# Performance work log

Hardware: AMD Instinct MI355X
Metric: run time of the kernel (lower is better)

The kernel has to match this reference:

```python
import jax, jax.numpy as jnp
import numpy as np

N = 8192
IN_F = 512
OUT_F = 512


def setup_inputs() -> dict:
    key = jax.random.key(0)
    k1, k2, k3, k4, k5 = jax.random.split(key, 5)
    scale = 1.0 / np.sqrt(IN_F)
    return {
        "embedding": jax.random.normal(k1, (N, IN_F), dtype=jnp.float32),
        "W_qk": jax.random.uniform(k2, (OUT_F, IN_F), dtype=jnp.float32, minval=-scale, maxval=scale),
        "b_qk": jax.random.uniform(k3, (OUT_F,), dtype=jnp.float32, minval=-scale, maxval=scale),
        "W_v": jax.random.uniform(k4, (OUT_F, IN_F), dtype=jnp.float32, minval=-scale, maxval=scale),
        "b_v": jax.random.uniform(k5, (OUT_F,), dtype=jnp.float32, minval=-scale, maxval=scale),
    }


def reference(embedding, W_qk, b_qk, W_v, b_v):
    # Q and K share the same projection (query_key Linear)
    Q = embedding @ W_qk.T + b_qk          # [N, D]
    K = Q                                   # identical projection
    V = embedding @ W_v.T + b_v             # [N, D]
    inv_sqrt_d = 1.0 / jnp.sqrt(jnp.asarray(OUT_F, dtype=embedding.dtype))
    scores = (Q @ K.T) * inv_sqrt_d         # [N, N]
    attn = jax.nn.softmax(scores, axis=1)   # row-wise softmax (dim=1)
    return attn @ V                         # [N, D]
```

## Files before the change

### kernel.cpp

```cpp
#include <hip/hip_runtime.h>
#include <hip/hip_bf16.h>


#define NTOK 8192
#define DIM  512

typedef unsigned short ushort_t;
typedef __attribute__((ext_vector_type(8))) __bf16 bf16x8;
typedef __attribute__((ext_vector_type(4))) float f32x4;

__device__ __forceinline__ float bf2f(ushort_t u) {
    union { unsigned int i; float f; } v; v.i = ((unsigned int)u) << 16; return v.f;
}
__device__ __forceinline__ ushort_t f2bf(float f) {
    union { float f; unsigned int i; } v; v.f = f;
    unsigned int b = v.i;
    return (ushort_t)((b + 0x7FFFu + ((b >> 16) & 1u)) >> 16);
}
__device__ __forceinline__ __bf16 f2bfh(float f) {
    union { ushort_t u; __bf16 h; } c; c.u = f2bf(f); return c.h;
}
__device__ __forceinline__ f32x4 mfma16(bf16x8 a, bf16x8 b, f32x4 c) {
    return __builtin_amdgcn_mfma_f32_16x16x32_bf16(a, b, c, 0, 0, 0);
}
__device__ __forceinline__ bf16x8 load8(const void* p, size_t idx, bool f32) {
    if (f32) {
        const float* f = (const float*)p + idx;
        bf16x8 r;
        #pragma unroll
        for (int j = 0; j < 8; ++j) r[j] = f2bfh(f[j]);
        return r;
    }
    return *(const bf16x8*)((const ushort_t*)p + idx);
}
__device__ __forceinline__ float loadS(const void* p, size_t idx, bool f32) {
    return f32 ? ((const float*)p)[idx] : bf2f(((const ushort_t*)p)[idx]);
}

#define LDA 520
#define LDP 264

__global__ void detect_kernel(const ushort_t* __restrict__ emb, int* __restrict__ flag)
{
    int lane = threadIdx.x;
    int cnt = 0;
    #pragma unroll
    for (int i = 0; i < 8; ++i) {
        ushort_t u = emb[(size_t)(lane * 8 + i) * 2];
        int a = u & 0x7FFF;
        int e = (u >> 7) & 0xFF;
        if (a == 0 || (e >= 111 && e <= 143)) cnt++;
    }
    cnt += __shfl_xor(cnt, 1);  cnt += __shfl_xor(cnt, 2);  cnt += __shfl_xor(cnt, 4);
    cnt += __shfl_xor(cnt, 8);  cnt += __shfl_xor(cnt, 16); cnt += __shfl_xor(cnt, 32);
    if (lane == 0) *flag = (cnt >= 460) ? 1 : 0;
}

__global__ __launch_bounds__(256)
void prep_kernel(const int* __restrict__ flag,
                 const void* __restrict__ Wqk, const void* __restrict__ bqk,
                 const void* __restrict__ Wv,  const void* __restrict__ bv,
                 ushort_t* __restrict__ Wqkb, ushort_t* __restrict__ bqkb,
                 ushort_t* __restrict__ Wvb,  ushort_t* __restrict__ bvb)
{
    const bool f32 = (*flag == 0);
    size_t gid = (size_t)blockIdx.x * 256 + threadIdx.x;
    size_t base = gid * 8;
    *(bf16x8*)&Wqkb[base] = load8(Wqk, base, f32);
    *(bf16x8*)&Wvb[base]  = load8(Wv,  base, f32);
    if (gid < 64) {
        *(bf16x8*)&bqkb[base] = load8(bqk, base, f32);
        *(bf16x8*)&bvb[base]  = load8(bv,  base, f32);
    }
}

__global__ __launch_bounds__(512)
void projqT_kernel(const int* __restrict__ flag, const void* __restrict__ emb,
                   const ushort_t* __restrict__ Wb, const ushort_t* __restrict__ bb,
                   ushort_t* __restrict__ C, ushort_t* __restrict__ embT)
{
    __shared__ ushort_t Alds[64][LDA];
    const bool f32 = (*flag == 0);
    const int tid  = threadIdx.x;
    const int wave = tid >> 6;
    const int lane = tid & 63;
    const int quad = lane >> 4;
    const int col  = lane & 15;
    const int mblk = blockIdx.x * 64;

    #pragma unroll
    for (int i = 0; i < 8; ++i) {
        int chunk = i * 512 + tid;
        int row = chunk >> 6;
        int k8  = (chunk & 63) * 8;
        *(bf16x8*)&Alds[row][k8] = load8(emb, (size_t)(mblk + row) * 512 + k8, f32);
    }
    __syncthreads();

    {
        ushort_t buf[64];
        #pragma unroll
        for (int r = 0; r < 64; ++r) buf[r] = Alds[r][tid];
        ushort_t* dst = embT + (size_t)tid * NTOK + mblk;
        #pragma unroll
        for (int i = 0; i < 8; ++i)
            *(uint4*)(dst + i * 8) = *(uint4*)&buf[i * 8];
    }

    f32x4 acc[4][4];
    #pragma unroll
    for (int r = 0; r < 4; ++r)
        #pragma unroll
        for (int c = 0; c < 4; ++c) acc[r][c] = (f32x4){0.f, 0.f, 0.f, 0.f};

    const int wcol = wave * 64;
    #pragma unroll
    for (int kk = 0; kk < 16; ++kk) {
        bf16x8 a[4];
        #pragma unroll
        for (int r = 0; r < 4; ++r)
            a[r] = *(const bf16x8*)&Alds[r * 16 + col][kk * 32 + quad * 8];
        #pragma unroll
        for (int c = 0; c < 4; ++c) {
            bf16x8 b = *(const bf16x8*)&Wb[(size_t)(wcol + c * 16 + col) * 512
                                           + kk * 32 + quad * 8];
            #pragma unroll
            for (int r = 0; r < 4; ++r)
                acc[r][c] = mfma16(a[r], b, acc[r][c]);
        }
    }

    #pragma unroll
    for (int r = 0; r < 4; ++r)
        #pragma unroll
        for (int c = 0; c < 4; ++c)
            #pragma unroll
            for (int g = 0; g < 4; ++g) {
                int m = mblk + r * 16 + quad * 4 + g;
                int n = wcol + c * 16 + col;
                C[(size_t)m * DIM + n] = f2bf(acc[r][c][g] + bf2f(bb[n]));
            }
}

__global__ __launch_bounds__(1024)
void attn64_kernel(const ushort_t* __restrict__ Q, const ushort_t* __restrict__ embT,
                   ushort_t* __restrict__ P0, ushort_t* __restrict__ P1,
                   float* __restrict__ lsumA)
{
    __shared__ ushort_t Qlds[64][LDA];
    __shared__ ushort_t Plds[2][64][LDP];
    __shared__ float    Lp[16][64];

    const int tid  = threadIdx.x;
    const int wave = tid >> 6;
    const int lane = tid & 63;
    const int quad = lane >> 4;
    const int col  = lane & 15;
    const int qt   = blockIdx.x & 127;
    const int ks   = blockIdx.x >> 7;
    const int q0   = qt * 64;
    const int kbase = ks * 4096;
    ushort_t* Ps = ks ? P1 : P0;

    #pragma unroll
    for (int i = 0; i < 4; ++i) {
        int chunk = i * 1024 + tid;
        int row = chunk >> 6;
        int k8  = (chunk & 63) * 8;
        *(bf16x8*)&Qlds[row][k8] = *(const bf16x8*)&Q[(size_t)(q0 + row) * 512 + k8];
    }
    __syncthreads();

    f32x4 accO[4][2];
    #pragma unroll
    for (int r = 0; r < 4; ++r)
        #pragma unroll
        for (int c = 0; c < 2; ++c) accO[r][c] = (f32x4){0.f, 0.f, 0.f, 0.f};

    float lsum[4][4];
    #pragma unroll
    for (int r = 0; r < 4; ++r)
        #pragma unroll
        for (int g = 0; g < 4; ++g) lsum[r][g] = 0.f;

    const float sc = 0.04419417382415922f * 1.4426950408889634f;
    const int wd = wave * 32;

    for (int it = 0; it < 16; ++it) {
        const int j0  = kbase + it * 256;
        const int buf = it & 1;

        f32x4 accS[4];
        #pragma unroll
        for (int r = 0; r < 4; ++r) accS[r] = (f32x4){0.f, 0.f, 0.f, 0.f};
        const size_t keyrow = (size_t)(j0 + wave * 16 + col) * 512;
        #pragma unroll
        for (int h = 0; h < 2; ++h) {
            bf16x8 kb[8];
            #pragma unroll
            for (int kk = 0; kk < 8; ++kk)
                kb[kk] = *(const bf16x8*)&Q[keyrow + (h * 8 + kk) * 32 + quad * 8];
            #pragma unroll
            for (int kk = 0; kk < 8; ++kk) {
                const int cofs = (h * 8 + kk) * 32 + quad * 8;
                #pragma unroll
                for (int r = 0; r < 4; ++r) {
                    bf16x8 a = *(const bf16x8*)&Qlds[r * 16 + col][cofs];
                    accS[r] = mfma16(a, kb[kk], accS[r]);
                }
            }
        }

        bf16x8 vbA[8];
        #pragma unroll
        for (int kk = 0; kk < 4; ++kk)
            #pragma unroll
            for (int c = 0; c < 2; ++c)
                vbA[kk * 2 + c] = *(const bf16x8*)&embT[
                    (size_t)(wd + c * 16 + col) * NTOK + j0 + kk * 32 + quad * 8];

        #pragma unroll
        for (int r = 0; r < 4; ++r)
            #pragma unroll
            for (int g = 0; g < 4; ++g) {
                float p = exp2f(fminf(accS[r][g] * sc, 126.0f));
                lsum[r][g] += p;
                Plds[buf][r * 16 + quad * 4 + g][wave * 16 + col] = f2bf(p);
            }

        bf16x8 vbB[8];
        #pragma unroll
        for (int kk = 0; kk < 4; ++kk)
            #pragma unroll
            for (int c = 0; c < 2; ++c)
                vbB[kk * 2 + c] = *(const bf16x8*)&embT[
                    (size_t)(wd + c * 16 + col) * NTOK + j0 + (4 + kk) * 32 + quad * 8];

        __syncthreads();

        #pragma unroll
        for (int kk = 0; kk < 4; ++kk) {
            #pragma unroll
            for (int r = 0; r < 4; ++r) {
                bf16x8 a = *(const bf16x8*)&Plds[buf][r * 16 + col][kk * 32 + quad * 8];
                #pragma unroll
                for (int c = 0; c < 2; ++c)
                    accO[r][c] = mfma16(a, vbA[kk * 2 + c], accO[r][c]);
            }
        }
        #pragma unroll
        for (int kk = 0; kk < 4; ++kk) {
            #pragma unroll
            for (int r = 0; r < 4; ++r) {
                bf16x8 a = *(const bf16x8*)&Plds[buf][r * 16 + col][(4 + kk) * 32 + quad * 8];
                #pragma unroll
                for (int c = 0; c < 2; ++c)
                    accO[r][c] = mfma16(a, vbB[kk * 2 + c], accO[r][c]);
            }
        }
    }

    #pragma unroll
    for (int r = 0; r < 4; ++r)
        #pragma unroll
        for (int g = 0; g < 4; ++g) {
            float s = lsum[r][g];
            s += __shfl_xor(s, 1);
            s += __shfl_xor(s, 2);
            s += __shfl_xor(s, 4);
            s += __shfl_xor(s, 8);
            if (col == 0)
                Lp[wave][r * 16 + quad * 4 + g] = s;
        }
    __syncthreads();
    if (tid < 64) {
        float t = 0.f;
        #pragma unroll
        for (int w = 0; w < 16; ++w) t += Lp[w][tid];
        lsumA[(size_t)ks * NTOK + q0 + tid] = t;
    }

    #pragma unroll
    for (int r = 0; r < 4; ++r)
        #pragma unroll
        for (int c = 0; c < 2; ++c)
            #pragma unroll
            for (int g = 0; g < 4; ++g)
                Ps[(size_t)(q0 + r * 16 + quad * 4 + g) * DIM + wd + c * 16 + col]
                    = f2bf(accO[r][c][g]);
}

__global__ __launch_bounds__(512)
void finalize_kernel(const int* __restrict__ flag,
                     const ushort_t* __restrict__ P0, const ushort_t* __restrict__ P1,
                     const float* __restrict__ lsumA,
                     const ushort_t* __restrict__ Wb, const ushort_t* __restrict__ bb,
                     void* __restrict__ Out)
{
    __shared__ ushort_t Alds[64][LDA];
    const bool f32 = (*flag == 0);
    const int tid  = threadIdx.x;
    const int wave = tid >> 6;
    const int lane = tid & 63;
    const int quad = lane >> 4;
    const int col  = lane & 15;
    const int mblk = blockIdx.x * 64;

    #pragma unroll
    for (int i = 0; i < 8; ++i) {
        int chunk = i * 512 + tid;
        int row = chunk >> 6;
        int k8  = (chunk & 63) * 8;
        int m   = mblk + row;
        float rv = 1.0f / (lsumA[m] + lsumA[NTOK + m]);
        bf16x8 v0 = *(const bf16x8*)&P0[(size_t)m * 512 + k8];
        bf16x8 v1 = *(const bf16x8*)&P1[(size_t)m * 512 + k8];
        bf16x8 t;
        #pragma unroll
        for (int j = 0; j < 8; ++j) t[j] = f2bfh(((float)v0[j] + (float)v1[j]) * rv);
        *(bf16x8*)&Alds[row][k8] = t;
    }
    __syncthreads();

    f32x4 acc[4][4];
    #pragma unroll
    for (int r = 0; r < 4; ++r)
        #pragma unroll
        for (int c = 0; c < 4; ++c) acc[r][c] = (f32x4){0.f, 0.f, 0.f, 0.f};

    const int wcol = wave * 64;
    #pragma unroll
    for (int kk = 0; kk < 16; ++kk) {
        bf16x8 a[4];
        #pragma unroll
        for (int r = 0; r < 4; ++r)
            a[r] = *(const bf16x8*)&Alds[r * 16 + col][kk * 32 + quad * 8];
        #pragma unroll
        for (int c = 0; c < 4; ++c) {
            bf16x8 b = *(const bf16x8*)&Wb[(size_t)(wcol + c * 16 + col) * 512
                                           + kk * 32 + quad * 8];
            #pragma unroll
            for (int r = 0; r < 4; ++r)
                acc[r][c] = mfma16(a[r], b, acc[r][c]);
        }
    }

    #pragma unroll
    for (int r = 0; r < 4; ++r)
        #pragma unroll
        for (int c = 0; c < 4; ++c)
            #pragma unroll
            for (int g = 0; g < 4; ++g) {
                int m = mblk + r * 16 + quad * 4 + g;
                int n = wcol + c * 16 + col;
                float v = acc[r][c][g] + bf2f(bb[n]);
                if (f32) ((float*)Out)[(size_t)m * DIM + n] = v;
                else     ((ushort_t*)Out)[(size_t)m * DIM + n] = f2bf(v);
            }
}

__global__ __launch_bounds__(256)
void transpose_kernel(const int* __restrict__ flag, const void* __restrict__ emb,
                      ushort_t* __restrict__ embT)
{
    __shared__ float tile[64][65];
    const bool f32 = (*flag == 0);
    const int t  = threadIdx.x;
    const int j0 = blockIdx.x * 64;
    const int d0 = blockIdx.y * 64;
    {
        int r = t >> 2, cs = (t & 3) * 16;
        if (f32) {
            const float* src = (const float*)emb + (size_t)(j0 + r) * DIM + d0 + cs;
            #pragma unroll
            for (int i = 0; i < 16; i += 4) {
                float4 v = *(const float4*)(src + i);
                tile[r][cs + i]     = v.x;
                tile[r][cs + i + 1] = v.y;
                tile[r][cs + i + 2] = v.z;
                tile[r][cs + i + 3] = v.w;
            }
        } else {
            const ushort_t* src = (const ushort_t*)emb + (size_t)(j0 + r) * DIM + d0 + cs;
            #pragma unroll
            for (int i = 0; i < 16; ++i) tile[r][cs + i] = bf2f(src[i]);
        }
    }
    __syncthreads();
    {
        int d = t >> 2, js = (t & 3) * 16;
        ushort_t buf[16];
        #pragma unroll
        for (int i = 0; i < 16; ++i) buf[i] = f2bf(tile[js + i][d]);
        ushort_t* dst = embT + (size_t)(d0 + d) * NTOK + j0 + js;
        *(uint4*)dst       = *(uint4*)&buf[0];
        *(uint4*)(dst + 8) = *(uint4*)&buf[8];
    }
}

__global__ __launch_bounds__(512)
void projq_kernel(const int* __restrict__ flag, const void* __restrict__ emb,
                  const void* __restrict__ W, const void* __restrict__ bias,
                  ushort_t* __restrict__ C)
{
    __shared__ ushort_t Alds[32][LDA];
    const bool f32 = (*flag == 0);
    const int tid  = threadIdx.x;
    const int wave = tid >> 6;
    const int lane = tid & 63;
    const int quad = lane >> 4;
    const int col  = lane & 15;
    const int mblk = blockIdx.x * 32;

    #pragma unroll
    for (int i = 0; i < 4; ++i) {
        int chunk = i * 512 + tid;
        int row = chunk >> 6;
        int k8  = (chunk & 63) * 8;
        *(bf16x8*)&Alds[row][k8] = load8(emb, (size_t)(mblk + row) * 512 + k8, f32);
    }
    __syncthreads();

    f32x4 acc[2][4];
    #pragma unroll
    for (int r = 0; r < 2; ++r)
        #pragma unroll
        for (int c = 0; c < 4; ++c) acc[r][c] = (f32x4){0.f, 0.f, 0.f, 0.f};

    const int wcol = wave * 64;
    #pragma unroll
    for (int kk = 0; kk < 16; ++kk) {
        bf16x8 a0 = *(const bf16x8*)&Alds[col][kk * 32 + quad * 8];
        bf16x8 a1 = *(const bf16x8*)&Alds[16 + col][kk * 32 + quad * 8];
        #pragma unroll
        for (int c = 0; c < 4; ++c) {
            bf16x8 b = load8(W, (size_t)(wcol + c * 16 + col) * 512 + kk * 32 + quad * 8, f32);
            acc[0][c] = mfma16(a0, b, acc[0][c]);
            acc[1][c] = mfma16(a1, b, acc[1][c]);
        }
    }

    #pragma unroll
    for (int r = 0; r < 2; ++r)
        #pragma unroll
        for (int c = 0; c < 4; ++c)
            #pragma unroll
            for (int g = 0; g < 4; ++g) {
                int m = mblk + r * 16 + quad * 4 + g;
                int n = wcol + c * 16 + col;
                C[(size_t)m * DIM + n] = f2bf(acc[r][c][g] + loadS(bias, n, f32));
            }
}

template <int VT>
__global__ __launch_bounds__(1024)
void attn_fused_kernel(const int* __restrict__ flag, const ushort_t* __restrict__ Q,
                       const void* __restrict__ embOrT, const void* __restrict__ Wv,
                       const void* __restrict__ bv, void* __restrict__ Out)
{
    __shared__ ushort_t Qlds[32][LDA];
    __shared__ ushort_t Plds[2][32][LDP];
    __shared__ float    Lpart[16][32];

    const bool f32 = (*flag == 0);
    const int tid  = threadIdx.x;
    const int wave = tid >> 6;
    const int lane = tid & 63;
    const int quad = lane >> 4;
    const int col  = lane & 15;
    const int q0   = blockIdx.x * 32;

    #pragma unroll
    for (int i = 0; i < 2; ++i) {
        int chunk = i * 1024 + tid;
        int row = chunk >> 6;
        int k8  = (chunk & 63) * 8;
        *(bf16x8*)&Qlds[row][k8] = *(const bf16x8*)&Q[(size_t)(q0 + row) * 512 + k8];
    }
    __syncthreads();

    f32x4 accO[2][2];
    #pragma unroll
    for (int r = 0; r < 2; ++r)
        #pragma unroll
        for (int c = 0; c < 2; ++c) accO[r][c] = (f32x4){0.f, 0.f, 0.f, 0.f};

    float lsum[2][4];
    #pragma unroll
    for (int r = 0; r < 2; ++r)
        #pragma unroll
        for (int g = 0; g < 4; ++g) lsum[r][g] = 0.f;

    const float sc = 0.04419417382415922f * 1.4426950408889634f;
    const int wOcol = wave * 32;

    for (int it = 0; it < 32; ++it) {
        const int j0  = it * 256;
        const int buf = it & 1;

        bf16x8 kb[16];
        const size_t keyrow = (size_t)(j0 + wave * 16 + col) * 512;
        #pragma unroll
        for (int kk = 0; kk < 16; ++kk)
            kb[kk] = *(const bf16x8*)&Q[keyrow + kk * 32 + quad * 8];

        f32x4 accS[2];
        accS[0] = (f32x4){0.f, 0.f, 0.f, 0.f};
        accS[1] = (f32x4){0.f, 0.f, 0.f, 0.f};
        #pragma unroll
        for (int kk = 0; kk < 16; ++kk) {
            bf16x8 a0 = *(const bf16x8*)&Qlds[col][kk * 32 + quad * 8];
            bf16x8 a1 = *(const bf16x8*)&Qlds[16 + col][kk * 32 + quad * 8];
            accS[0] = mfma16(a0, kb[kk], accS[0]);
            accS[1] = mfma16(a1, kb[kk], accS[1]);
        }

        bf16x8 vb[16];
        #pragma unroll
        for (int kk = 0; kk < 8; ++kk)
            #pragma unroll
            for (int c = 0; c < 2; ++c) {
                if (VT) {
                    vb[kk * 2 + c] = *(const bf16x8*)((const ushort_t*)embOrT
                        + (size_t)(wOcol + c * 16 + col) * NTOK + j0 + kk * 32 + quad * 8);
                } else {
                    size_t base = (size_t)(j0 + kk * 32 + quad * 8) * 512 + (wOcol + c * 16 + col);
                    bf16x8 b;
                    if (f32) {
                        const float* bp = (const float*)embOrT + base;
                        #pragma unroll
                        for (int j = 0; j < 8; ++j) b[j] = f2bfh(bp[(size_t)j * 512]);
                    } else {
                        const __bf16* bp = (const __bf16*)embOrT + base;
                        #pragma unroll
                        for (int j = 0; j < 8; ++j) b[j] = bp[(size_t)j * 512];
                    }
                    vb[kk * 2 + c] = b;
                }
            }

        #pragma unroll
        for (int r = 0; r < 2; ++r)
            #pragma unroll
            for (int g = 0; g < 4; ++g) {
                float p = exp2f(fminf(accS[r][g] * sc, 126.0f));
                lsum[r][g] += p;
                Plds[buf][r * 16 + quad * 4 + g][wave * 16 + col] = f2bf(p);
            }

        __syncthreads();

        #pragma unroll
        for (int kk = 0; kk < 8; ++kk) {
            bf16x8 a0 = *(const bf16x8*)&Plds[buf][col][kk * 32 + quad * 8];
            bf16x8 a1 = *(const bf16x8*)&Plds[buf][16 + col][kk * 32 + quad * 8];
            #pragma unroll
            for (int c = 0; c < 2; ++c) {
                accO[0][c] = mfma16(a0, vb[kk * 2 + c], accO[0][c]);
                accO[1][c] = mfma16(a1, vb[kk * 2 + c], accO[1][c]);
            }
        }
    }

    #pragma unroll
    for (int r = 0; r < 2; ++r)
        #pragma unroll
        for (int g = 0; g < 4; ++g) {
            float s = lsum[r][g];
            s += __shfl_xor(s, 1);
            s += __shfl_xor(s, 2);
            s += __shfl_xor(s, 4);
            s += __shfl_xor(s, 8);
            lsum[r][g] = s;
        }
    if (col == 0) {
        #pragma unroll
        for (int r = 0; r < 2; ++r)
            #pragma unroll
            for (int g = 0; g < 4; ++g)
                Lpart[wave][r * 16 + quad * 4 + g] = lsum[r][g];
    }
    __syncthreads();

    #pragma unroll
    for (int r = 0; r < 2; ++r) {
        float rinv[4];
        #pragma unroll
        for (int g = 0; g < 4; ++g) {
            float t = 0.f;
            #pragma unroll
            for (int w = 0; w < 16; ++w) t += Lpart[w][r * 16 + quad * 4 + g];
            rinv[g] = 1.0f / t;
        }
        #pragma unroll
        for (int c = 0; c < 2; ++c)
            #pragma unroll
            for (int g = 0; g < 4; ++g)
                Qlds[r * 16 + quad * 4 + g][wOcol + c * 16 + col] = f2bf(accO[r][c][g] * rinv[g]);
    }
    __syncthreads();

    f32x4 acc2[2][2];
    #pragma unroll
    for (int r = 0; r < 2; ++r)
        #pragma unroll
        for (int c = 0; c < 2; ++c) acc2[r][c] = (f32x4){0.f, 0.f, 0.f, 0.f};

    #pragma unroll
    for (int kk = 0; kk < 16; ++kk) {
        bf16x8 a0 = *(const bf16x8*)&Qlds[col][kk * 32 + quad * 8];
        bf16x8 a1 = *(const bf16x8*)&Qlds[16 + col][kk * 32 + quad * 8];
        #pragma unroll
        for (int c = 0; c < 2; ++c) {
            bf16x8 b = load8(Wv, (size_t)(wOcol + c * 16 + col) * 512 + kk * 32 + quad * 8, f32);
            acc2[0][c] = mfma16(a0, b, acc2[0][c]);
            acc2[1][c] = mfma16(a1, b, acc2[1][c]);
        }
    }

    #pragma unroll
    for (int r = 0; r < 2; ++r)
        #pragma unroll
        for (int c = 0; c < 2; ++c)
            #pragma unroll
            for (int g = 0; g < 4; ++g) {
                int m = q0 + r * 16 + quad * 4 + g;
                int n = wOcol + c * 16 + col;
                float v = acc2[r][c][g] + loadS(bv, n, f32);
                if (f32) ((float*)Out)[(size_t)m * DIM + n] = v;
                else     ((ushort_t*)Out)[(size_t)m * DIM + n] = f2bf(v);
            }
}

extern "C" void kernel_launch(void* const* d_in, const int* in_sizes, int n_in,
                              void* d_out, int out_size, void* d_ws, size_t ws_size,
                              hipStream_t stream)
{
    const void* emb = d_in[0];
    const void* Wqk = d_in[1];
    const void* bqk = d_in[2];
    const void* Wv  = d_in[3];
    const void* bv  = d_in[4];

    char* W = (char*)d_ws;
    int*      flag  = (int*)W;
    float*    lsumA = (float*)(W + 64);
    ushort_t* Wqkb  = (ushort_t*)(W + 64 + 65536);
    ushort_t* Wvb   = Wqkb + (size_t)DIM * DIM;
    ushort_t* bqkb  = Wvb + (size_t)DIM * DIM;
    ushort_t* bvb   = bqkb + DIM;
    ushort_t* embT  = bvb + DIM;
    ushort_t* Qws   = embT + (size_t)DIM * NTOK;
    ushort_t* P0    = Qws + (size_t)DIM * NTOK;
    ushort_t* P1    = P0 + (size_t)NTOK * DIM;

    const size_t needA = 64 + 65536 + 2 * (size_t)DIM * DIM * 2 + 2 * DIM * 2
                       + 4 * (size_t)NTOK * DIM * 2;
    const size_t needB = 64 + 2 * (size_t)NTOK * DIM * 2;

    detect_kernel<<<dim3(1), dim3(64), 0, stream>>>((const ushort_t*)emb, flag);

    if (ws_size >= needA) {
        prep_kernel<<<dim3(128), dim3(256), 0, stream>>>(flag, Wqk, bqk, Wv, bv,
                                                         Wqkb, bqkb, Wvb, bvb);
        projqT_kernel<<<dim3(NTOK / 64), dim3(512), 0, stream>>>(flag, emb, Wqkb, bqkb,
                                                                 Qws, embT);
        attn64_kernel<<<dim3(256), dim3(1024), 0, stream>>>(Qws, embT, P0, P1, lsumA);
        finalize_kernel<<<dim3(NTOK / 64), dim3(512), 0, stream>>>(flag, P0, P1, lsumA,
                                                                   Wvb, bvb, d_out);
    } else if (ws_size >= needB) {
        ushort_t* embT2 = (ushort_t*)(W + 64);
        ushort_t* Qws2  = embT2 + (size_t)DIM * NTOK;
        transpose_kernel<<<dim3(128, 8), dim3(256), 0, stream>>>(flag, emb, embT2);
        projq_kernel<<<dim3(NTOK / 32), dim3(512), 0, stream>>>(flag, emb, Wqk, bqk, Qws2);
        attn_fused_kernel<1><<<dim3(NTOK / 32), dim3(1024), 0, stream>>>(
            flag, Qws2, embT2, Wv, bv, d_out);
    } else {
        ushort_t* Qsm = (ushort_t*)(W + 64);
        projq_kernel<<<dim3(NTOK / 32), dim3(512), 0, stream>>>(flag, emb, Wqk, bqk, Qsm);
        attn_fused_kernel<0><<<dim3(NTOK / 32), dim3(1024), 0, stream>>>(
            flag, Qsm, emb, Wv, bv, d_out);
    }
}
```

Baseline: 382.7 us.

## Add 128-row query tile attention with 4-way key split and async K loads

Adds a new attention kernel that processes 128 query rows per block with 512 threads, splits the keys four ways across blocks, and double-buffers K tiles into shared memory via global_load_lds with an XOR swizzle. Q fragments stay in registers and V is read directly from the transposed embedding. A new finalize kernel sums the four partial outputs and the row sums, then applies the V projection. This aims to raise reuse of each K/V tile and overlap loads with MFMA work, at the cost of a larger workspace and more partial-output traffic. The path only runs when the workspace is large enough, otherwise the older paths are used.

Result: slower. 641.7 us (+67.7%).

```diff
diff --git a/kernel.cpp b/kernel.cpp
--- a/kernel.cpp
+++ b/kernel.cpp
@@ -6,6 +6,7 @@
 #define DIM  512
 
 typedef unsigned short ushort_t;
+typedef unsigned int u32;
 typedef __attribute__((ext_vector_type(8))) __bf16 bf16x8;
 typedef __attribute__((ext_vector_type(4))) float f32x4;
 
@@ -35,6 +36,11 @@
 }
 __device__ __forceinline__ float loadS(const void* p, size_t idx, bool f32) {
     return f32 ? ((const float*)p)[idx] : bf2f(((const ushort_t*)p)[idx]);
+}
+__device__ __forceinline__ void gload_lds16(const ushort_t* g, ushort_t* l) {
+    __builtin_amdgcn_global_load_lds(
+        (const __attribute__((address_space(1))) u32*)g,
+        (__attribute__((address_space(3))) u32*)l, 16, 0, 0);
 }
 
 #define LDA 520
@@ -139,6 +145,247 @@
                 int m = mblk + r * 16 + quad * 4 + g;
                 int n = wcol + c * 16 + col;
                 C[(size_t)m * DIM + n] = f2bf(acc[r][c][g] + bf2f(bb[n]));
+            }
+}
+
+#define QT   128
+#define KTI  64
+#define NITR 32
+
+__global__ __launch_bounds__(512, 2)
+void attn128_kernel(const ushort_t* __restrict__ Q, const ushort_t* __restrict__ embT,
+                    ushort_t* __restrict__ P, float* __restrict__ lsumA)
+{
+    __shared__ ushort_t Klds[2][KTI * DIM];
+    __shared__ ushort_t Plds[QT * KTI];
+
+    const int tid  = threadIdx.x;
+    const int wave = tid >> 6;
+    const int lane = tid & 63;
+    const int quad = lane >> 4;
+    const int col  = lane & 15;
+    const int qt   = blockIdx.x & 63;
+    const int ks   = blockIdx.x >> 6;
+    const int q0   = qt * QT;
+    const int kbase = ks * (NTOK / 4);
+    ushort_t* Ps = P + (size_t)ks * NTOK * DIM;
+
+    bf16x8 qf[16];
+    {
+        const ushort_t* qrow = Q + (size_t)(q0 + wave * 16 + col) * DIM + quad * 8;
+        #pragma unroll
+        for (int kk = 0; kk < 16; ++kk)
+            qf[kk] = *(const bf16x8*)(qrow + kk * 32);
+    }
+
+    {
+        const size_t base = (size_t)kbase * DIM;
+        #pragma unroll
+        for (int i = 0; i < 8; ++i) {
+            const int r = wave * 8 + i;
+            const int sw = (r ^ (r >> 3)) & 7;
+            gload_lds16(Q + base + (size_t)r * DIM + ((lane ^ sw) << 3),
+                        &Klds[0][r * DIM]);
+        }
+    }
+
+    f32x4 accO[8][4];
+    #pragma unroll
+    for (int r = 0; r < 8; ++r)
+        #pragma unroll
+        for (int c = 0; c < 4; ++c) accO[r][c] = (f32x4){0.f, 0.f, 0.f, 0.f};
+    float lsum[4] = {0.f, 0.f, 0.f, 0.f};
+
+    const float sc = 0.04419417382415922f * 1.4426950408889634f;
+    const int wd = wave * 64;
+
+    int rb[4], sx[4];
+    #pragma unroll
+    for (int kt = 0; kt < 4; ++kt) {
+        const int r = kt * 16 + col;
+        const int sw = (r ^ (r >> 3)) & 7;
+        rb[kt] = r * DIM + ((quad ^ (sw & 3)) << 3);
+        sx[kt] = (sw & 4) << 3;
+    }
+    int pb[8], px[8];
+    #pragma unroll
+    for (int rt = 0; rt < 8; ++rt) {
+        const int r = rt * 16 + col;
+        const int sw = (r ^ (r >> 3)) & 7;
+        pb[rt] = r * KTI + ((quad ^ (sw & 3)) << 3);
+        px[rt] = (sw & 4) << 3;
+    }
+    int pw[4], pwx[4];
+    #pragma unroll
+    for (int g = 0; g < 4; ++g) {
+        const int row = wave * 16 + quad * 4 + g;
+        const int sw = (row ^ (row >> 3)) & 7;
+        pw[g]  = row * KTI;
+        pwx[g] = sw << 3;
+    }
+
+    __syncthreads();
+
+    for (int it = 0; it < NITR; ++it) {
+        const int cur = it & 1;
+        const ushort_t* Kc = &Klds[cur][0];
+        const int j0 = kbase + it * KTI;
+
+        if (it + 1 < NITR) {
+            const size_t base = (size_t)(j0 + KTI) * DIM;
+            ushort_t* dst = &Klds[cur ^ 1][0];
+            #pragma unroll
+            for (int i = 0; i < 8; ++i) {
+                const int r = wave * 8 + i;
+                const int sw = (r ^ (r >> 3)) & 7;
+                gload_lds16(Q + base + (size_t)r * DIM + ((lane ^ sw) << 3),
+                            dst + r * DIM);
+            }
+        }
+
+        f32x4 accS[4];
+        #pragma unroll
+        for (int kt = 0; kt < 4; ++kt) accS[kt] = (f32x4){0.f, 0.f, 0.f, 0.f};
+        __builtin_amdgcn_s_setprio(1);
+        #pragma unroll
+        for (int kk = 0; kk < 16; ++kk)
+            #pragma unroll
+            for (int kt = 0; kt < 4; ++kt) {
+                bf16x8 kb = *(const bf16x8*)&Kc[rb[kt] + ((kk << 5) ^ sx[kt])];
+                accS[kt] = mfma16(qf[kk], kb, accS[kt]);
+            }
+        __builtin_amdgcn_s_setprio(0);
+
+        bf16x8 vA[4], vB[4];
+        {
+            const ushort_t* eb = embT + (size_t)(wd + col) * NTOK + j0 + quad * 8;
+            #pragma unroll
+            for (int dt = 0; dt < 4; ++dt) {
+                vA[dt] = *(const bf16x8*)(eb + (size_t)(dt * 16) * NTOK);
+                vB[dt] = *(const bf16x8*)(eb + (size_t)(dt * 16) * NTOK + 32);
+            }
+        }
+
+        #pragma unroll
+        for (int kt = 0; kt < 4; ++kt)
+            #pragma unroll
+            for (int g = 0; g < 4; ++g) {
+                float p = exp2f(fminf(accS[kt][g] * sc, 126.0f));
+                lsum[g] += p;
+                Plds[pw[g] + ((kt * 16 + col) ^ pwx[g])] = f2bf(p);
+            }
+
+        asm volatile("s_waitcnt lgkmcnt(0)" ::: "memory");
+        __builtin_amdgcn_s_barrier();
+
+        __builtin_amdgcn_s_setprio(1);
+        #pragma unroll
+        for (int rt = 0; rt < 8; ++rt) {
+            bf16x8 pa0 = *(const bf16x8*)&Plds[pb[rt] + px[rt]];
+            bf16x8 pa1 = *(const bf16x8*)&Plds[pb[rt] + (32 ^ px[rt])];
+            #pragma unroll
+            for (int dt = 0; dt < 4; ++dt) {
+                accO[rt][dt] = mfma16(pa0, vA[dt], accO[rt][dt]);
+                accO[rt][dt] = mfma16(pa1, vB[dt], accO[rt][dt]);
+            }
+        }
+        __builtin_amdgcn_s_setprio(0);
+
+        __syncthreads();
+    }
+
+    #pragma unroll
+    for (int g = 0; g < 4; ++g) {
+        float s = lsum[g];
+        s += __shfl_xor(s, 1);
+        s += __shfl_xor(s, 2);
+        s += __shfl_xor(s, 4);
+        s += __shfl_xor(s, 8);
+        if (col == 0)
+            lsumA[(size_t)ks * NTOK + q0 + wave * 16 + quad * 4 + g] = s;
+    }
+
+    #pragma unroll
+    for (int rt = 0; rt < 8; ++rt)
+        #pragma unroll
+        for (int dt = 0; dt < 4; ++dt)
+            #pragma unroll
+            for (int g = 0; g < 4; ++g)
+                Ps[(size_t)(q0 + rt * 16 + quad * 4 + g) * DIM + wd + dt * 16 + col]
+                    = f2bf(accO[rt][dt][g]);
+}
+
+__global__ __launch_bounds__(512)
+void finalize4_kernel(const int* __restrict__ flag,
+                      const ushort_t* __restrict__ P, const float* __restrict__ lsumA,
+                      const ushort_t* __restrict__ Wb, const ushort_t* __restrict__ bb,
+                      void* __restrict__ Out)
+{
+    __shared__ ushort_t Alds[64][LDA];
+    const bool f32 = (*flag == 0);
+    const int tid  = threadIdx.x;
+    const int wave = tid >> 6;
+    const int lane = tid & 63;
+    const int quad = lane >> 4;
+    const int col  = lane & 15;
+    const int mblk = blockIdx.x * 64;
+    const size_t PSZ = (size_t)NTOK * DIM;
+
+    #pragma unroll
+    for (int i = 0; i < 8; ++i) {
+        int chunk = i * 512 + tid;
+        int row = chunk >> 6;
+        int k8  = (chunk & 63) * 8;
+        int m   = mblk + row;
+        float rv = 1.0f / (lsumA[m] + lsumA[NTOK + m]
+                         + lsumA[2 * NTOK + m] + lsumA[3 * NTOK + m]);
+        size_t off = (size_t)m * 512 + k8;
+        bf16x8 v0 = *(const bf16x8*)&P[off];
+        bf16x8 v1 = *(const bf16x8*)&P[PSZ + off];
+        bf16x8 v2 = *(const bf16x8*)&P[2 * PSZ + off];
+        bf16x8 v3 = *(const bf16x8*)&P[3 * PSZ + off];
+        bf16x8 t;
+        #pragma unroll
+        for (int j = 0; j < 8; ++j)
+            t[j] = f2bfh(((float)v0[j] + (float)v1[j] + (float)v2[j] + (float)v3[j]) * rv);
+        *(bf16x8*)&Alds[row][k8] = t;
+    }
+    __syncthreads();
+
+    f32x4 acc[4][4];
+    #pragma unroll
+    for (int r = 0; r < 4; ++r)
+        #pragma unroll
+        for (int c = 0; c < 4; ++c) acc[r][c] = (f32x4){0.f, 0.f, 0.f, 0.f};
+
+    const int wcol = wave * 64;
+    #pragma unroll
+    for (int kk = 0; kk < 16; ++kk) {
+        bf16x8 a[4];
+        #pragma unroll
+        for (int r = 0; r < 4; ++r)
+            a[r] = *(const bf16x8*)&Alds[r * 16 + col][kk * 32 + quad * 8];
+        #pragma unroll
+        for (int c = 0; c < 4; ++c) {
+            bf16x8 b = *(const bf16x8*)&Wb[(size_t)(wcol + c * 16 + col) * 512
+                                           + kk * 32 + quad * 8];
+            #pragma unroll
+            for (int r = 0; r < 4; ++r)
+                acc[r][c] = mfma16(a[r], b, acc[r][c]);
+        }
+    }
+
+    #pragma unroll
+    for (int r = 0; r < 4; ++r)
+        #pragma unroll
+        for (int c = 0; c < 4; ++c)
+            #pragma unroll
+            for (int g = 0; g < 4; ++g) {
+                int m = mblk + r * 16 + quad * 4 + g;
+                int n = wcol + c * 16 + col;
+                float v = acc[r][c][g] + bf2f(bb[n]);
+                if (f32) ((float*)Out)[(size_t)m * DIM + n] = v;
+                else     ((ushort_t*)Out)[(size_t)m * DIM + n] = f2bf(v);
             }
 }
 
@@ -643,24 +890,44 @@
     const void* bv  = d_in[4];
 
     char* W = (char*)d_ws;
-    int*      flag  = (int*)W;
-    float*    lsumA = (float*)(W + 64);
-    ushort_t* Wqkb  = (ushort_t*)(W + 64 + 65536);
-    ushort_t* Wvb   = Wqkb + (size_t)DIM * DIM;
-    ushort_t* bqkb  = Wvb + (size_t)DIM * DIM;
-    ushort_t* bvb   = bqkb + DIM;
-    ushort_t* embT  = bvb + DIM;
-    ushort_t* Qws   = embT + (size_t)DIM * NTOK;
-    ushort_t* P0    = Qws + (size_t)DIM * NTOK;
-    ushort_t* P1    = P0 + (size_t)NTOK * DIM;
-
+    int* flag = (int*)W;
+
+    const size_t needC = 64 + 4 * (size_t)NTOK * 4 + 2 * (size_t)DIM * DIM * 2
+                       + 2 * DIM * 2 + 6 * (size_t)NTOK * DIM * 2;
     const size_t needA = 64 + 65536 + 2 * (size_t)DIM * DIM * 2 + 2 * DIM * 2
                        + 4 * (size_t)NTOK * DIM * 2;
     const size_t needB = 64 + 2 * (size_t)NTOK * DIM * 2;
 
     detect_kernel<<<dim3(1), dim3(64), 0, stream>>>((const ushort_t*)emb, flag);
 
-    if (ws_size >= needA) {
+    if (ws_size >= needC) {
+        float*    lsum4 = (float*)(W + 64);
+        ushort_t* Wqkb  = (ushort_t*)(W + 64 + 4 * (size_t)NTOK * 4);
+        ushort_t* Wvb   = Wqkb + (size_t)DIM * DIM;
+        ushort_t* bqkb  = Wvb + (size_t)DIM * DIM;
+        ushort_t* bvb   = bqkb + DIM;
+        ushort_t* embT  = bvb + DIM;
+        ushort_t* Qws   = embT + (size_t)DIM * NTOK;
+        ushort_t* P4    = Qws + (size_t)DIM * NTOK;
+
+        prep_kernel<<<dim3(128), dim3(256), 0, stream>>>(flag, Wqk, bqk, Wv, bv,
+                                                         Wqkb, bqkb, Wvb, bvb);
+        projqT_kernel<<<dim3(NTOK / 64), dim3(512), 0, stream>>>(flag, emb, Wqkb, bqkb,
+                                                                 Qws, embT);
+        attn128_kernel<<<dim3(256), dim3(512), 0, stream>>>(Qws, embT, P4, lsum4);
+        finalize4_kernel<<<dim3(NTOK / 64), dim3(512), 0, stream>>>(flag, P4, lsum4,
+                                                                    Wvb, bvb, d_out);
+    } else if (ws_size >= needA) {
+        float*    lsumA = (float*)(W + 64);
+        ushort_t* Wqkb  = (ushort_t*)(W + 64 + 65536);
+        ushort_t* Wvb   = Wqkb + (size_t)DIM * DIM;
+        ushort_t* bqkb  = Wvb + (size_t)DIM * DIM;
+        ushort_t* bvb   = bqkb + DIM;
+        ushort_t* embT  = bvb + DIM;
+        ushort_t* Qws   = embT + (size_t)DIM * NTOK;
+        ushort_t* P0    = Qws + (size_t)DIM * NTOK;
+        ushort_t* P1    = P0 + (size_t)NTOK * DIM;
+
         prep_kernel<<<dim3(128), dim3(256), 0, stream>>>(flag, Wqk, bqk, Wv, bv,
                                                          Wqkb, bqkb, Wvb, bvb);
         projqT_kernel<<<dim3(NTOK / 64), dim3(512), 0, stream>>>(flag, emb, Wqkb, bqkb,
```
